# Performance work log

Hardware: AMD Instinct MI355X
Metric: run time of the kernel (lower is better)

Reference implementation:

```python
import jax, jax.numpy as jnp
import numpy as np

B, T, D, V = 64, 2048, 64, 100000


def create_beta_stack(feats, times):
    """feats: [F,B,T] float, times: [B,T] float.
    beta[:, :, i] = (times[:,i]-times[:,i-1] + mask_{i-1} * beta[:,:,i-1]) * (times[:,i] != -1)
    where mask = (feat != -1) & (feat != 0). Sequential reset/accumulate scan over T."""
    dt = times[:, 1:] - times[:, :-1]                                   # [B, T-1]
    mask = ((feats[:, :, :-1] != -1) & (feats[:, :, :-1] != 0)).astype(feats.dtype)  # [F,B,T-1]
    pad = (times[:, 1:] != -1).astype(feats.dtype)                      # [B, T-1]

    def step(b, xs):
        dt_i, m_i, p_i = xs                      # [B], [F,B], [B]
        b_new = (dt_i[None, :] + m_i * b) * p_i[None, :]
        return b_new, b_new

    init = jnp.zeros(feats.shape[:2], feats.dtype)                      # [F,B]
    _, betas = jax.lax.scan(step, init, (dt.T, jnp.moveaxis(mask, 2, 0), pad.T))  # [T-1,F,B]
    beta = jnp.concatenate([init[None], betas], axis=0)                 # [T,F,B]
    return jnp.moveaxis(beta, 0, 2)                                     # [F,B,T]


def setup_inputs() -> dict:
    key = jax.random.key(0)
    ks = jax.random.split(key, 11)
    cat1 = jax.random.randint(ks[0], (B, T), 0, V)
    cat2 = jax.random.randint(ks[1], (B, T), 0, V)
    num1 = jax.random.normal(ks[2], (B, T), jnp.float32)
    num2 = jax.random.normal(ks[3], (B, T), jnp.float32)
    # integer-valued, sorted per row (event timestamps); no -1 padding
    event_time = jnp.sort(jax.random.randint(ks[4], (B, T), 0, 10000), axis=1).astype(jnp.float32)
    E1 = jax.random.normal(ks[5], (V, D), jnp.float32) * 0.02
    E2 = jax.random.normal(ks[6], (V, D), jnp.float32) * 0.02
    w1 = jax.random.normal(ks[7], (D,), jnp.float32) * 0.02
    b1 = jax.random.normal(ks[8], (D,), jnp.float32) * 0.02
    w2 = jax.random.normal(ks[9], (D,), jnp.float32) * 0.02
    b2 = jax.random.normal(ks[10], (D,), jnp.float32) * 0.02
    return {"cat1": cat1, "cat2": cat2, "num1": num1, "num2": num2,
            "event_time": event_time, "E1": E1, "E2": E2,
            "w1": w1, "b1": b1, "w2": w2, "b2": b2}


def reference(cat1, cat2, num1, num2, event_time, E1, E2, w1, b1, w2, b2):
    times = event_time.astype(jnp.float32)
    # categorical embeddings [B,T,D]
    emb1 = E1[cat1]
    emb2 = E2[cat2]
    # numeric Linear(1, D): values[...,None] @ W.T + b
    nemb1 = num1[..., None] * w1 + b1
    nemb2 = num2[..., None] * w2 + b2
    # time-since-last-valid-event recurrence, stacked over all 4 features
    feats = jnp.stack([cat1.astype(jnp.float32), cat2.astype(jnp.float32), num1, num2], axis=0)  # [4,B,T]
    betas = create_beta_stack(feats, times)                             # [4,B,T]
    rep = lambda x: jnp.broadcast_to(x[..., None], x.shape + (D,))
    delta = jnp.concatenate([rep(betas[0]), rep(betas[1]), rep(betas[2]), rep(betas[3])], axis=-1)  # [B,T,4D]
    m = lambda v: rep((v != -1) & (v != 0))
    mask = jnp.concatenate([m(cat1), m(cat2), m(num1), m(num2)], axis=-1)  # [B,T,4D] bool
    features = jnp.concatenate([emb1, emb2, nemb1, nemb2], axis=-1)     # [B,T,4D]
    return (features, times, delta, mask)
```

## Files before the change

kernel.cpp:

```cpp
#include <hip/hip_runtime.h>

#define BB 64
#define TT 2048
#define DD 64
#define BT (BB * TT)
#define OFF_F 0
#define OFF_T (BT * 256)
#define OFF_D (OFF_T + BT)
#define OFF_M (OFF_D + BT * 256)

typedef float v4f __attribute__((ext_vector_type(4)));

__device__ __forceinline__ void nt_store4(float* p, float x, float y, float z, float w) {
    v4f v = {x, y, z, w};
    __builtin_nontemporal_store(v, (v4f*)p);
}
__device__ __forceinline__ void nt_store4v(float* p, float4 v) {
    nt_store4(p, v.x, v.y, v.z, v.w);
}

__global__ __launch_bounds__(64) void beta_scan_kernel(
    const int* __restrict__ cat1, const int* __restrict__ cat2,
    const float* __restrict__ num1, const float* __restrict__ num2,
    const float* __restrict__ times, float* __restrict__ beta_ws)
{
    const int f    = blockIdx.x >> 6;
    const int b    = blockIdx.x & 63;
    const int lane = threadIdx.x;
    const int lo   = lane * 32;

    const float* trow = times + b * TT;

    float t[32], v[32];
    {
        const float4* t4 = (const float4*)(trow + lo);
        #pragma unroll
        for (int q = 0; q < 8; ++q) {
            float4 x = t4[q];
            t[4*q+0] = x.x; t[4*q+1] = x.y; t[4*q+2] = x.z; t[4*q+3] = x.w;
        }
    }
    if (f < 2) {
        const int* crow = (f == 0 ? cat1 : cat2) + b * TT;
        const int4* c4 = (const int4*)(crow + lo);
        #pragma unroll
        for (int q = 0; q < 8; ++q) {
            int4 x = c4[q];
            v[4*q+0] = (float)x.x; v[4*q+1] = (float)x.y;
            v[4*q+2] = (float)x.z; v[4*q+3] = (float)x.w;
        }
    } else {
        const float* nrow = (f == 2 ? num1 : num2) + b * TT;
        const float4* n4 = (const float4*)(nrow + lo);
        #pragma unroll
        for (int q = 0; q < 8; ++q) {
            float4 x = n4[q];
            v[4*q+0] = x.x; v[4*q+1] = x.y; v[4*q+2] = x.z; v[4*q+3] = x.w;
        }
    }
    float tprev = 0.f, vprev = 0.f;
    if (lane > 0) {
        tprev = trow[lo - 1];
        if      (f == 0) vprev = (float)cat1[b * TT + lo - 1];
        else if (f == 1) vprev = (float)cat2[b * TT + lo - 1];
        else if (f == 2) vprev = num1[b * TT + lo - 1];
        else             vprev = num2[b * TT + lo - 1];
    }

    float A = 1.f, C = 0.f;
    #pragma unroll
    for (int k = 0; k < 32; ++k) {
        float a, c;
        if (lo + k == 0) { a = 0.f; c = 0.f; }
        else {
            float ti  = t[k];
            float tp  = (k == 0) ? tprev : t[k-1];
            float fv  = (k == 0) ? vprev : v[k-1];
            float pad = (ti != -1.f) ? 1.f : 0.f;
            float m   = (fv != -1.f && fv != 0.f) ? 1.f : 0.f;
            a = m * pad;
            c = (ti - tp) * pad;
        }
        C = a * C + c;
        A = A * a;
    }
    for (int d = 1; d < 64; d <<= 1) {
        float Ap = __shfl_up(A, d);
        float Cp = __shfl_up(C, d);
        if (lane >= d) { C = A * Cp + C; A = A * Ap; }
    }
    float beta = __shfl_up(C, 1);
    if (lane == 0) beta = 0.f;

    float* out = beta_ws + (size_t)b * TT * 4 + f;
    #pragma unroll
    for (int k = 0; k < 32; ++k) {
        float a, c;
        if (lo + k == 0) { a = 0.f; c = 0.f; }
        else {
            float ti  = t[k];
            float tp  = (k == 0) ? tprev : t[k-1];
            float fv  = (k == 0) ? vprev : v[k-1];
            float pad = (ti != -1.f) ? 1.f : 0.f;
            float m   = (fv != -1.f && fv != 0.f) ? 1.f : 0.f;
            a = m * pad;
            c = (ti - tp) * pad;
        }
        beta = a * beta + c;
        out[(lo + k) * 4] = beta;
    }
}

__global__ __launch_bounds__(256) void expand_kernel(
    const int* __restrict__ cat1, const int* __restrict__ cat2,
    const float* __restrict__ num1, const float* __restrict__ num2,
    const float* __restrict__ times,
    const float* __restrict__ E1, const float* __restrict__ E2,
    const float* __restrict__ w1, const float* __restrict__ b1,
    const float* __restrict__ w2, const float* __restrict__ b2,
    const float* __restrict__ beta_ws, float* __restrict__ out)
{
    const int u    = blockIdx.x * 256 + threadIdx.x;
    const int lane = threadIdx.x & 63;
    const int wid  = __builtin_amdgcn_readfirstlane((int)(threadIdx.x >> 6));
    const int bt0  = (blockIdx.x << 4) | (wid << 2);
    const int q    = lane >> 4;
    const int c    = lane & 15;

    const int4   i1v = *(const int4*)(cat1 + bt0);
    const int4   i2v = *(const int4*)(cat2 + bt0);
    const float4 x1v = *(const float4*)(num1 + bt0);
    const float4 x2v = *(const float4*)(num2 + bt0);
    const float4 be0 = ((const float4*)beta_ws)[bt0 + 0];
    const float4 be1 = ((const float4*)beta_ws)[bt0 + 1];
    const float4 be2 = ((const float4*)beta_ws)[bt0 + 2];
    const float4 be3 = ((const float4*)beta_ws)[bt0 + 3];

    const float* s0 = (q == 0) ? E1 + (size_t)i1v.x * DD
                   : (q == 1) ? E2 + (size_t)i2v.x * DD
                   : (q == 2) ? w1 : w2;
    const float* s1 = (q == 0) ? E1 + (size_t)i1v.y * DD
                   : (q == 1) ? E2 + (size_t)i2v.y * DD
                   : (q == 2) ? w1 : w2;
    const float* s2 = (q == 0) ? E1 + (size_t)i1v.z * DD
                   : (q == 1) ? E2 + (size_t)i2v.z * DD
                   : (q == 2) ? w1 : w2;
    const float* s3 = (q == 0) ? E1 + (size_t)i1v.w * DD
                   : (q == 1) ? E2 + (size_t)i2v.w * DD
                   : (q == 2) ? w1 : w2;

    const float4 a0 = ((const float4*)s0)[c];
    const float4 a1 = ((const float4*)s1)[c];
    const float4 a2 = ((const float4*)s2)[c];
    const float4 a3 = ((const float4*)s3)[c];
    const float4 bb = ((const float4*)((q == 3) ? b2 : b1))[c];

#define EMIT_TOKEN(J, AJ, BEJ, I1, I2, X1, X2)                                  \
    {                                                                           \
        const float x  = (q == 3) ? (X2) : (X1);                                \
        float4 val;                                                             \
        val.x = (q < 2) ? (AJ).x : fmaf(x, (AJ).x, bb.x);                       \
        val.y = (q < 2) ? (AJ).y : fmaf(x, (AJ).y, bb.y);                       \
        val.z = (q < 2) ? (AJ).z : fmaf(x, (AJ).z, bb.z);                       \
        val.w = (q < 2) ? (AJ).w : fmaf(x, (AJ).w, bb.w);                       \
        const float m1 = ((I1) != -1   && (I1) != 0  ) ? 1.f : 0.f;             \
        const float m2 = ((I2) != -1   && (I2) != 0  ) ? 1.f : 0.f;             \
        const float m3 = ((X1) != -1.f && (X1) != 0.f) ? 1.f : 0.f;             \
        const float m4 = ((X2) != -1.f && (X2) != 0.f) ? 1.f : 0.f;             \
        const float m  = (q == 0) ? m1 : (q == 1) ? m2 : (q == 2) ? m3 : m4;    \
        const float bv = (q == 0) ? (BEJ).x : (q == 1) ? (BEJ).y                \
                       : (q == 2) ? (BEJ).z : (BEJ).w;                          \
        const size_t o = ((size_t)(bt0 + (J)) << 6) | (size_t)lane;             \
        nt_store4v(out + OFF_F + (o << 2), val);                                \
        nt_store4 (out + OFF_D + (o << 2), bv, bv, bv, bv);                     \
        nt_store4 (out + OFF_M + (o << 2), m, m, m, m);                         \
    }

    EMIT_TOKEN(0, a0, be0, i1v.x, i2v.x, x1v.x, x2v.x)
    EMIT_TOKEN(1, a1, be1, i1v.y, i2v.y, x1v.y, x2v.y)
    EMIT_TOKEN(2, a2, be2, i1v.z, i2v.z, x1v.z, x2v.z)
    EMIT_TOKEN(3, a3, be3, i1v.w, i2v.w, x1v.w, x2v.w)
#undef EMIT_TOKEN

    if (u < BT / 4) {
        float4 t = ((const float4*)times)[u];
        nt_store4v(out + OFF_T + 4 * u, t);
    }
}

extern "C" void kernel_launch(void* const* d_in, const int* in_sizes, int n_in,
                              void* d_out, int out_size, void* d_ws, size_t ws_size,
                              hipStream_t stream) {
    const int*   cat1  = (const int*)d_in[0];
    const int*   cat2  = (const int*)d_in[1];
    const float* num1  = (const float*)d_in[2];
    const float* num2  = (const float*)d_in[3];
    const float* times = (const float*)d_in[4];
    const float* E1    = (const float*)d_in[5];
    const float* E2    = (const float*)d_in[6];
    const float* w1    = (const float*)d_in[7];
    const float* b1    = (const float*)d_in[8];
    const float* w2    = (const float*)d_in[9];
    const float* b2    = (const float*)d_in[10];
    float* out     = (float*)d_out;
    float* beta_ws = (float*)d_ws;

    beta_scan_kernel<<<4 * BB, 64, 0, stream>>>(cat1, cat2, num1, num2, times, beta_ws);

    expand_kernel<<<BT / 16, 256, 0, stream>>>(
        cat1, cat2, num1, num2, times, E1, E2, w1, b1, w2, b2, beta_ws, out);
}
```

Before: 458.0 us.

## Split fused expand kernel into separate feature, delta and mask kernels

Breaks the single expand kernel into three kernels: one writes the embedding features and times, one broadcasts beta into the delta output, and one computes and broadcasts the mask. The aim is simpler per-kernel store streams and fewer live registers in each kernel. In exchange there are two extra kernel launches, the index arrays are re-read, and the three output streams are no longer written together.

```diff
diff --git a/kernel.cpp b/kernel.cpp
--- a/kernel.cpp
+++ b/kernel.cpp
@@ -111,14 +111,14 @@
     }
 }
 
-__global__ __launch_bounds__(256) void expand_kernel(
+__global__ __launch_bounds__(256) void feat_kernel(
     const int* __restrict__ cat1, const int* __restrict__ cat2,
     const float* __restrict__ num1, const float* __restrict__ num2,
     const float* __restrict__ times,
     const float* __restrict__ E1, const float* __restrict__ E2,
     const float* __restrict__ w1, const float* __restrict__ b1,
     const float* __restrict__ w2, const float* __restrict__ b2,
-    const float* __restrict__ beta_ws, float* __restrict__ out)
+    float* __restrict__ out)
 {
     const int u    = blockIdx.x * 256 + threadIdx.x;
     const int lane = threadIdx.x & 63;
@@ -131,10 +131,6 @@
     const int4   i2v = *(const int4*)(cat2 + bt0);
     const float4 x1v = *(const float4*)(num1 + bt0);
     const float4 x2v = *(const float4*)(num2 + bt0);
-    const float4 be0 = ((const float4*)beta_ws)[bt0 + 0];
-    const float4 be1 = ((const float4*)beta_ws)[bt0 + 1];
-    const float4 be2 = ((const float4*)beta_ws)[bt0 + 2];
-    const float4 be3 = ((const float4*)beta_ws)[bt0 + 3];
 
     const float* s0 = (q == 0) ? E1 + (size_t)i1v.x * DD
                    : (q == 1) ? E2 + (size_t)i2v.x * DD
@@ -155,7 +151,7 @@
     const float4 a3 = ((const float4*)s3)[c];
     const float4 bb = ((const float4*)((q == 3) ? b2 : b1))[c];
 
-#define EMIT_TOKEN(J, AJ, BEJ, I1, I2, X1, X2)                                  \
+#define EMIT_F(J, AJ, X1, X2)                                                   \
     {                                                                           \
         const float x  = (q == 3) ? (X2) : (X1);                                \
         float4 val;                                                             \
@@ -163,29 +159,49 @@
         val.y = (q < 2) ? (AJ).y : fmaf(x, (AJ).y, bb.y);                       \
         val.z = (q < 2) ? (AJ).z : fmaf(x, (AJ).z, bb.z);                       \
         val.w = (q < 2) ? (AJ).w : fmaf(x, (AJ).w, bb.w);                       \
-        const float m1 = ((I1) != -1   && (I1) != 0  ) ? 1.f : 0.f;             \
-        const float m2 = ((I2) != -1   && (I2) != 0  ) ? 1.f : 0.f;             \
-        const float m3 = ((X1) != -1.f && (X1) != 0.f) ? 1.f : 0.f;             \
-        const float m4 = ((X2) != -1.f && (X2) != 0.f) ? 1.f : 0.f;             \
-        const float m  = (q == 0) ? m1 : (q == 1) ? m2 : (q == 2) ? m3 : m4;    \
-        const float bv = (q == 0) ? (BEJ).x : (q == 1) ? (BEJ).y                \
-                       : (q == 2) ? (BEJ).z : (BEJ).w;                          \
         const size_t o = ((size_t)(bt0 + (J)) << 6) | (size_t)lane;             \
         nt_store4v(out + OFF_F + (o << 2), val);                                \
-        nt_store4 (out + OFF_D + (o << 2), bv, bv, bv, bv);                     \
-        nt_store4 (out + OFF_M + (o << 2), m, m, m, m);                         \
-    }
-
-    EMIT_TOKEN(0, a0, be0, i1v.x, i2v.x, x1v.x, x2v.x)
-    EMIT_TOKEN(1, a1, be1, i1v.y, i2v.y, x1v.y, x2v.y)
-    EMIT_TOKEN(2, a2, be2, i1v.z, i2v.z, x1v.z, x2v.z)
-    EMIT_TOKEN(3, a3, be3, i1v.w, i2v.w, x1v.w, x2v.w)
-#undef EMIT_TOKEN
+    }
+
+    EMIT_F(0, a0, x1v.x, x2v.x)
+    EMIT_F(1, a1, x1v.y, x2v.y)
+    EMIT_F(2, a2, x1v.z, x2v.z)
+    EMIT_F(3, a3, x1v.w, x2v.w)
+#undef EMIT_F
 
     if (u < BT / 4) {
         float4 t = ((const float4*)times)[u];
         nt_store4v(out + OFF_T + 4 * u, t);
     }
+}
+
+__global__ __launch_bounds__(256) void delta_kernel(
+    const float* __restrict__ beta_ws, float* __restrict__ out)
+{
+    const int g     = blockIdx.x * 256 + threadIdx.x;
+    const int token = g >> 6;
+    const int f     = (g >> 4) & 3;
+    const float bv  = beta_ws[token * 4 + f];
+    nt_store4(out + OFF_D + ((size_t)g << 2), bv, bv, bv, bv);
+}
+
+__global__ __launch_bounds__(256) void mask_kernel(
+    const int* __restrict__ cat1, const int* __restrict__ cat2,
+    const float* __restrict__ num1, const float* __restrict__ num2,
+    float* __restrict__ out)
+{
+    const int g     = blockIdx.x * 256 + threadIdx.x;
+    const int token = g >> 6;
+    const int f     = (g >> 4) & 3;
+    float m;
+    if (f < 2) {
+        const int i = (f == 0) ? cat1[token] : cat2[token];
+        m = (i != -1 && i != 0) ? 1.f : 0.f;
+    } else {
+        const float x = (f == 2) ? num1[token] : num2[token];
+        m = (x != -1.f && x != 0.f) ? 1.f : 0.f;
+    }
+    nt_store4(out + OFF_M + ((size_t)g << 2), m, m, m, m);
 }
 
 extern "C" void kernel_launch(void* const* d_in, const int* in_sizes, int n_in,
@@ -207,6 +223,8 @@
 
     beta_scan_kernel<<<4 * BB, 64, 0, stream>>>(cat1, cat2, num1, num2, times, beta_ws);
 
-    expand_kernel<<<BT / 16, 256, 0, stream>>>(
-        cat1, cat2, num1, num2, times, E1, E2, w1, b1, w2, b2, beta_ws, out);
-}
+    feat_kernel<<<BT / 16, 256, 0, stream>>>(
+        cat1, cat2, num1, num2, times, E1, E2, w1, b1, w2, b2, out);
+    delta_kernel<<<(BT * 64) / 256, 256, 0, stream>>>(beta_ws, out);
+    mask_kernel<<<(BT * 64) / 256, 256, 0, stream>>>(cat1, cat2, num1, num2, out);
+}
```

Measured after the change: 450.9 us. About the same (-1.6%).
